# Performance work log

Hardware: AMD Instinct MI355X
Metric: run time of the kernel (lower is better)

The kernel has to match this reference:

```python
import jax, jax.numpy as jnp
import numpy as np

B, Q, K, F, H, D = 2, 4096, 4096, 512, 8, 64

def setup_inputs() -> dict:
    key = jax.random.key(0)
    ks = jax.random.split(key, 6)
    s = 1.0 / np.sqrt(F)
    return {
        "inputs_q": jax.random.normal(ks[0], (B, Q, F), dtype=jnp.float32),
        "inputs_kv": jax.random.normal(ks[1], (B, K, F), dtype=jnp.float32),
        "Wq": jax.random.normal(ks[2], (F, H, D), dtype=jnp.float32) * s,
        "Wk": jax.random.normal(ks[3], (F, H, D), dtype=jnp.float32) * s,
        "Wv": jax.random.normal(ks[4], (F, H, D), dtype=jnp.float32) * s,
        "Wo": jax.random.normal(ks[5], (H, D, F), dtype=jnp.float32) * (1.0 / np.sqrt(H * D)),
    }

def reference(inputs_q, inputs_kv, Wq, Wk, Wv, Wo):
    # QKV projections (DenseGeneral, no bias): [B, L, F] -> [B, L, H, D]
    q = jnp.einsum("bqf,fhd->bqhd", inputs_q, Wq)
    k = jnp.einsum("bkf,fhd->bkhd", inputs_kv, Wk)
    v = jnp.einsum("bkf,fhd->bkhd", inputs_kv, Wv)
    # Explicit attention matrix [B, H, Q, K] as in the original module
    logits = jnp.einsum("bqhd,bkhd->bhqk", q, k)
    attn = jax.nn.softmax(logits, axis=-1)
    out = jnp.einsum("bhqk,bkhd->bqhd", attn, v)
    # Output projection over (heads, head_dim): [B, Q, H, D] -> [B, Q, F]
    return jnp.einsum("bqhd,hdf->bqf", out, Wo)
```

## Files before the change

### kernel.cpp

```cpp
#include <hip/hip_runtime.h>
#include <hip/hip_bf16.h>

typedef short bf16x8 __attribute__((ext_vector_type(8)));
typedef _Float16 f16;
typedef f16 f16x8 __attribute__((ext_vector_type(8)));
typedef float f32x4 __attribute__((ext_vector_type(4)));
typedef unsigned short u16;
typedef u16 u16x8 __attribute__((ext_vector_type(8)));
typedef unsigned int u32;
typedef u32 u32x2 __attribute__((ext_vector_type(2)));

#define B_  2
#define L_  4096
#define F_  512
#define H_  8
#define D_  64
#define M_  8192
#define NSPL 2
#define KHALF (L_ / NSPL)

#define LOG2E 1.442695041f

__device__ inline u16 f2bf(float f) {
    union { float f; unsigned u; } v; v.f = f;
    unsigned r = v.u + 0x7fff + ((v.u >> 16) & 1);
    return (u16)(r >> 16);
}
__device__ inline u16 f2h(float f) {
    union { f16 h; u16 u; } v; v.h = (f16)f;
    return v.u;
}
__device__ inline float h2f(u16 u) {
    union { u16 u; f16 h; } v; v.u = u;
    return (float)v.h;
}

__global__ __launch_bounds__(256) void wt_kernel(
    const float* __restrict__ Wq, const float* __restrict__ Wk,
    const float* __restrict__ Wv, const float* __restrict__ Wo,
    u16* __restrict__ Tq, u16* __restrict__ Tk,
    u16* __restrict__ Tv, u16* __restrict__ To) {
    __shared__ float t[32][33];
    const int z = blockIdx.z;
    const float* in = (z == 0) ? Wq : (z == 1) ? Wk : (z == 2) ? Wv : Wo;
    u16* out = (z == 0) ? Tq : (z == 1) ? Tk : (z == 2) ? Tv : To;
    int k0 = blockIdx.y * 32, n0 = blockIdx.x * 32;
    int c = threadIdx.x & 31, r8 = threadIdx.x >> 5;
#pragma unroll
    for (int i = 0; i < 4; ++i) {
        int r = r8 * 4 + i;
        t[r][c] = in[(size_t)(k0 + r) * F_ + n0 + c];
    }
    __syncthreads();
#pragma unroll
    for (int i = 0; i < 4; ++i) {
        int r = r8 * 4 + i;
        out[(size_t)(n0 + r) * F_ + k0 + c] = f2h(t[c][r]);
    }
}

__global__ __launch_bounds__(256, 3) void proj_kernel(
    const float* __restrict__ Xq, const float* __restrict__ Xkv,
    const u16* __restrict__ Wqt, const u16* __restrict__ Wkt,
    const u16* __restrict__ Wvt,
    u16* __restrict__ Qw, u16* __restrict__ Kw, u16* __restrict__ Vw) {
    __shared__ u16 Ah[128][72];
    __shared__ u16 B1[64][72];
    __shared__ u16 B2[64][72];
    const int tid = threadIdx.x;
    const int w = tid >> 6, lane = tid & 63, lx = lane & 15, quad = lane >> 4;
    const int m0 = blockIdx.y * 128, n0 = blockIdx.x * 64;
    const bool isKV = (blockIdx.z == 1);
    const float* A = isKV ? Xkv : Xq;
    const u16* W1 = isKV ? Wkt : Wqt;

    float4 apre[8];
    u16x8 b1p[2], b2p[2];

    auto load_ab = [&](int k0) {
#pragma unroll
        for (int it = 0; it < 4; ++it) {
            int slot = tid + it * 256, r = slot >> 3, g = (slot & 7) * 8;
            apre[2 * it]     = *(const float4*)(A + (size_t)(m0 + r) * F_ + k0 + g);
            apre[2 * it + 1] = *(const float4*)(A + (size_t)(m0 + r) * F_ + k0 + g + 4);
        }
#pragma unroll
        for (int it = 0; it < 2; ++it) {
            int slot = tid + it * 256, r = slot >> 3, g = (slot & 7) * 8;
            b1p[it] = *(const u16x8*)(W1 + (size_t)(n0 + r) * F_ + k0 + g);
            if (isKV)
                b2p[it] = *(const u16x8*)(Wvt + (size_t)(n0 + r) * F_ + k0 + g);
        }
    };
    auto write_ab = [&]() {
#pragma unroll
        for (int it = 0; it < 4; ++it) {
            int slot = tid + it * 256, r = slot >> 3, g = (slot & 7) * 8;
            float4 f0 = apre[2 * it], f1 = apre[2 * it + 1];
            u16 th[8] = {f2h(f0.x), f2h(f0.y), f2h(f0.z), f2h(f0.w),
                         f2h(f1.x), f2h(f1.y), f2h(f1.z), f2h(f1.w)};
            *(u16x8*)&Ah[r][g] = *(u16x8*)th;
        }
#pragma unroll
        for (int it = 0; it < 2; ++it) {
            int slot = tid + it * 256, r = slot >> 3, g = (slot & 7) * 8;
            *(u16x8*)&B1[r][g] = b1p[it];
            if (isKV) *(u16x8*)&B2[r][g] = b2p[it];
        }
    };

    f32x4 acc1[2][4] = {}, acc2[2][4] = {};

    load_ab(0);
    write_ab();
    __syncthreads();
    load_ab(64);

    for (int k0 = 0; k0 < F_; k0 += 64) {
#pragma unroll
        for (int ks = 0; ks < 2; ++ks) {
            f16x8 af[2];
#pragma unroll
            for (int mf = 0; mf < 2; ++mf)
                af[mf] = *(const f16x8*)&Ah[w * 32 + mf * 16 + lx][ks * 32 + quad * 8];
#pragma unroll
            for (int nt = 0; nt < 4; ++nt) {
                f16x8 b1 = *(const f16x8*)&B1[nt * 16 + lx][ks * 32 + quad * 8];
#pragma unroll
                for (int mf = 0; mf < 2; ++mf)
                    acc1[mf][nt] = __builtin_amdgcn_mfma_f32_16x16x32_f16(af[mf], b1, acc1[mf][nt], 0, 0, 0);
                if (isKV) {
                    f16x8 b2 = *(const f16x8*)&B2[nt * 16 + lx][ks * 32 + quad * 8];
#pragma unroll
                    for (int mf = 0; mf < 2; ++mf)
                        acc2[mf][nt] = __builtin_amdgcn_mfma_f32_16x16x32_f16(af[mf], b2, acc2[mf][nt], 0, 0, 0);
                }
            }
        }
        if (k0 < F_ - 64) {
            __syncthreads();
            write_ab();
            __syncthreads();
            if (k0 < F_ - 128) load_ab(k0 + 128);
        }
    }

    const int h = n0 >> 6;
    const float scl = isKV ? 1.0f : LOG2E;
    u16* C1 = isKV ? Kw : Qw;
#pragma unroll
    for (int mf = 0; mf < 2; ++mf)
#pragma unroll
        for (int nt = 0; nt < 4; ++nt)
#pragma unroll
            for (int i = 0; i < 4; ++i) {
                int m = m0 + w * 32 + mf * 16 + quad * 4 + i;
                int b = m >> 12, l = m & 4095;
                int d = nt * 16 + lx;
                C1[((size_t)(b * H_ + h) * L_ + l) * D_ + d] = f2h(acc1[mf][nt][i] * scl);
            }
    if (isKV) {
        __syncthreads();
#pragma unroll
        for (int mf = 0; mf < 2; ++mf)
#pragma unroll
            for (int nt = 0; nt < 4; ++nt)
#pragma unroll
                for (int i = 0; i < 4; ++i)
                    Ah[w * 32 + mf * 16 + quad * 4 + i][nt * 16 + lx] = f2bf(acc2[mf][nt][i]);
        __syncthreads();
        int d = tid >> 2, seg = (tid & 3) * 32;
        int b = m0 >> 12;
        u16 tmp[32];
#pragma unroll
        for (int j = 0; j < 32; ++j) tmp[j] = Ah[seg + j][d];
        size_t base = ((size_t)(b * H_ + h) * D_ + d) * L_ + (m0 & 4095) + seg;
#pragma unroll
        for (int c = 0; c < 4; ++c)
            *(u16x8*)(Vw + base + c * 8) = *(u16x8*)&tmp[c * 8];
    }
}

__global__ __launch_bounds__(256) void out_gemm(const u16* __restrict__ A16,
                                                const u16* __restrict__ Wt,
                                                float* __restrict__ Cf) {
    __shared__ u16 As[128][72];
    __shared__ u16 Bs[64][72];
    const int tid = threadIdx.x;
    const int w = tid >> 6, lane = tid & 63, lx = lane & 15, quad = lane >> 4;
    const int m0 = blockIdx.y * 128, n0 = blockIdx.x * 64;

    u16x8 a16p[4];
    u16x8 bp[2];

    auto load_ab = [&](int k0) {
#pragma unroll
        for (int it = 0; it < 4; ++it) {
            int slot = tid + it * 256, r = slot >> 3, g = (slot & 7) * 8;
            a16p[it] = *(const u16x8*)(A16 + (size_t)(m0 + r) * F_ + k0 + g);
        }
#pragma unroll
        for (int it = 0; it < 2; ++it) {
            int slot = tid + it * 256, r = slot >> 3, g = (slot & 7) * 8;
            bp[it] = *(const u16x8*)(Wt + (size_t)(n0 + r) * F_ + k0 + g);
        }
    };
    auto write_ab = [&]() {
#pragma unroll
        for (int it = 0; it < 4; ++it) {
            int slot = tid + it * 256, r = slot >> 3, g = (slot & 7) * 8;
            *(u16x8*)&As[r][g] = a16p[it];
        }
#pragma unroll
        for (int it = 0; it < 2; ++it) {
            int slot = tid + it * 256, r = slot >> 3, g = (slot & 7) * 8;
            *(u16x8*)&Bs[r][g] = bp[it];
        }
    };

    f32x4 acc[2][4] = {};

    load_ab(0);
    write_ab();
    __syncthreads();
    load_ab(64);

    for (int k0 = 0; k0 < F_; k0 += 64) {
#pragma unroll
        for (int ks = 0; ks < 2; ++ks) {
            f16x8 af[2];
#pragma unroll
            for (int mf = 0; mf < 2; ++mf)
                af[mf] = *(const f16x8*)&As[w * 32 + mf * 16 + lx][ks * 32 + quad * 8];
#pragma unroll
            for (int nt = 0; nt < 4; ++nt) {
                f16x8 bf = *(const f16x8*)&Bs[nt * 16 + lx][ks * 32 + quad * 8];
#pragma unroll
                for (int mf = 0; mf < 2; ++mf)
                    acc[mf][nt] = __builtin_amdgcn_mfma_f32_16x16x32_f16(af[mf], bf, acc[mf][nt], 0, 0, 0);
            }
        }
        if (k0 < F_ - 64) {
            __syncthreads();
            write_ab();
            __syncthreads();
            if (k0 < F_ - 128) load_ab(k0 + 128);
        }
    }

#pragma unroll
    for (int mf = 0; mf < 2; ++mf)
#pragma unroll
        for (int nt = 0; nt < 4; ++nt)
#pragma unroll
            for (int i = 0; i < 4; ++i) {
                int m = m0 + w * 32 + mf * 16 + quad * 4 + i;
                int n = n0 + nt * 16 + lx;
                Cf[(size_t)m * F_ + n] = acc[mf][nt][i];
            }
}

__global__ __launch_bounds__(256, 2) void flash_mfma(
    const u16* __restrict__ Qg, const u16* __restrict__ Kg,
    const u16* __restrict__ Vtg, u16* __restrict__ On, float* __restrict__ Ls) {
    __shared__ u16 Ks[2][64][72];
    __shared__ u16 Vs[2][64][72];

    const int tid = threadIdx.x;
    const int w = tid >> 6, lane = tid & 63, lx = lane & 15, quad = lane >> 4;

    const int x = blockIdx.x;
    const int t = x >> 3;
    const int hh = t >> 5;
    const int s = (t >> 4) & 1;
    const int bh = (x & 7) * 2 + hh;
    const int q0 = (t & 15) * 256;

    const u16* Qp = Qg + ((size_t)bh * L_ + q0) * D_;
    const u16* Kp = Kg + (size_t)bh * L_ * D_ + (size_t)(s * KHALF) * D_;
    const u16* Vp = Vtg + (size_t)bh * D_ * L_ + s * KHALF;

    f16x8 qreg[4][2];
#pragma unroll
    for (int qf = 0; qf < 4; ++qf)
#pragma unroll
        for (int ks = 0; ks < 2; ++ks)
            qreg[qf][ks] = *(const f16x8*)(Qp + (size_t)(w * 64 + qf * 16 + lx) * D_ +
                                           ks * 32 + quad * 8);

    u16x8 kp[2], vp[2];
    auto load_kv = [&](int kt) {
#pragma unroll
        for (int it = 0; it < 2; ++it) {
            int slot = tid + it * 256, r = slot >> 3, g = (slot & 7) * 8;
            kp[it] = *(const u16x8*)(Kp + (size_t)(kt * 64 + r) * D_ + g);
            vp[it] = *(const u16x8*)(Vp + (size_t)r * L_ + kt * 64 + g);
        }
    };
    auto write_kv = [&](int p) {
#pragma unroll
        for (int it = 0; it < 2; ++it) {
            int slot = tid + it * 256, r = slot >> 3, g = (slot & 7) * 8;
            *(u16x8*)&Ks[p][r][g] = kp[it];
            *(u16x8*)&Vs[p][r][g] = vp[it];
        }
    };

    const bf16x8 vone = {0x3F80, 0x3F80, 0x3F80, 0x3F80,
                         0x3F80, 0x3F80, 0x3F80, 0x3F80};
    f32x4 o[4][4] = {};
    f32x4 osum[4] = {};

    load_kv(0);
    write_kv(0);
    __syncthreads();
    load_kv(1);

    const int NT = KHALF / 64;
    for (int kt = 0; kt < NT; ++kt) {
        const int p = kt & 1;

        f32x4 sv[2][4] = {};
#pragma unroll
        for (int ks = 0; ks < 2; ++ks)
#pragma unroll
            for (int nt = 0; nt < 2; ++nt) {
                f16x8 ak = *(const f16x8*)&Ks[p][nt * 16 + lx][ks * 32 + quad * 8];
#pragma unroll
                for (int qf = 0; qf < 4; ++qf)
                    sv[nt][qf] = __builtin_amdgcn_mfma_f32_16x16x32_f16(ak, qreg[qf][ks], sv[nt][qf], 0, 0, 0);
            }

        if (kt < NT - 1) write_kv(p ^ 1);

        bf16x8 ap0[4];
#pragma unroll
        for (int qf = 0; qf < 4; ++qf) {
            u32 pu[2], pw[2];
#pragma unroll
            for (int nt = 0; nt < 2; ++nt) {
                u32 ub[4];
#pragma unroll
                for (int i = 0; i < 4; ++i)
                    ub[i] = __float_as_uint(__builtin_amdgcn_exp2f(sv[nt][qf][i]));
                pu[nt] = __builtin_amdgcn_perm(ub[1], ub[0], 0x07060302u);
                pw[nt] = __builtin_amdgcn_perm(ub[3], ub[2], 0x07060302u);
            }
            u32x2 r  = __builtin_amdgcn_permlane32_swap(pu[0], pu[1], false, false);
            u32x2 r2 = __builtin_amdgcn_permlane16_swap(r[0], r[1], false, false);
            u32x2 tt = __builtin_amdgcn_permlane32_swap(pw[0], pw[1], false, false);
            u32x2 t2 = __builtin_amdgcn_permlane16_swap(tt[0], tt[1], false, false);
            union { u32 d[4]; bf16x8 h; } cvt;
            cvt.d[0] = r2[0];
            cvt.d[1] = t2[0];
            cvt.d[2] = r2[1];
            cvt.d[3] = t2[1];
            ap0[qf] = cvt.h;
        }

        __builtin_amdgcn_s_setprio(1);
#pragma unroll
        for (int qf = 0; qf < 4; ++qf)
            osum[qf] = __builtin_amdgcn_mfma_f32_16x16x32_bf16(ap0[qf], vone, osum[qf], 0, 0, 0);
#pragma unroll
        for (int nt = 0; nt < 4; ++nt) {
            bf16x8 bv = *(const bf16x8*)&Vs[p][nt * 16 + lx][quad * 8];
#pragma unroll
            for (int qf = 0; qf < 4; ++qf)
                o[qf][nt] = __builtin_amdgcn_mfma_f32_16x16x32_bf16(ap0[qf], bv, o[qf][nt], 0, 0, 0);
        }
        __builtin_amdgcn_s_setprio(0);

#pragma unroll
        for (int nt = 0; nt < 2; ++nt)
#pragma unroll
            for (int qf = 0; qf < 4; ++qf)
                sv[nt][qf] = (f32x4){0.f, 0.f, 0.f, 0.f};
#pragma unroll
        for (int ks = 0; ks < 2; ++ks)
#pragma unroll
            for (int nt = 0; nt < 2; ++nt) {
                f16x8 ak = *(const f16x8*)&Ks[p][(nt + 2) * 16 + lx][ks * 32 + quad * 8];
#pragma unroll
                for (int qf = 0; qf < 4; ++qf)
                    sv[nt][qf] = __builtin_amdgcn_mfma_f32_16x16x32_f16(ak, qreg[qf][ks], sv[nt][qf], 0, 0, 0);
            }

        bf16x8 ap1[4];
#pragma unroll
        for (int qf = 0; qf < 4; ++qf) {
            u32 pu[2], pw[2];
#pragma unroll
            for (int nt = 0; nt < 2; ++nt) {
                u32 ub[4];
#pragma unroll
                for (int i = 0; i < 4; ++i)
                    ub[i] = __float_as_uint(__builtin_amdgcn_exp2f(sv[nt][qf][i]));
                pu[nt] = __builtin_amdgcn_perm(ub[1], ub[0], 0x07060302u);
                pw[nt] = __builtin_amdgcn_perm(ub[3], ub[2], 0x07060302u);
            }
            u32x2 r  = __builtin_amdgcn_permlane32_swap(pu[0], pu[1], false, false);
            u32x2 r2 = __builtin_amdgcn_permlane16_swap(r[0], r[1], false, false);
            u32x2 tt = __builtin_amdgcn_permlane32_swap(pw[0], pw[1], false, false);
            u32x2 t2 = __builtin_amdgcn_permlane16_swap(tt[0], tt[1], false, false);
            union { u32 d[4]; bf16x8 h; } cvt;
            cvt.d[0] = r2[0];
            cvt.d[1] = t2[0];
            cvt.d[2] = r2[1];
            cvt.d[3] = t2[1];
            ap1[qf] = cvt.h;
        }

        __builtin_amdgcn_s_setprio(1);
#pragma unroll
        for (int qf = 0; qf < 4; ++qf)
            osum[qf] = __builtin_amdgcn_mfma_f32_16x16x32_bf16(ap1[qf], vone, osum[qf], 0, 0, 0);
#pragma unroll
        for (int nt = 0; nt < 4; ++nt) {
            bf16x8 bv = *(const bf16x8*)&Vs[p][nt * 16 + lx][32 + quad * 8];
#pragma unroll
            for (int qf = 0; qf < 4; ++qf)
                o[qf][nt] = __builtin_amdgcn_mfma_f32_16x16x32_bf16(ap1[qf], bv, o[qf][nt], 0, 0, 0);
        }
        __builtin_amdgcn_s_setprio(0);

        if (kt < NT - 2) load_kv(kt + 2);
        if (kt < NT - 1) __syncthreads();
    }

    const int b = bh >> 3, h = bh & 7;
    u16* Op = On + (size_t)s * M_ * F_;
#pragma unroll
    for (int qf = 0; qf < 4; ++qf) {
        float linv[4];
#pragma unroll
        for (int i = 0; i < 4; ++i) linv[i] = 1.f / osum[qf][i];
#pragma unroll
        for (int nt = 0; nt < 4; ++nt)
#pragma unroll
            for (int i = 0; i < 4; ++i) {
                int l = q0 + w * 64 + qf * 16 + quad * 4 + i;
                Op[((size_t)b * L_ + l) * (H_ * D_) + h * D_ + nt * 16 + lx] =
                    f2h(o[qf][nt][i] * linv[i]);
            }
        if (lx == 0) {
            float* lp = Ls + ((size_t)s * (B_ * H_) + bh) * L_ +
                        q0 + w * 64 + qf * 16 + quad * 4;
#pragma unroll
            for (int i = 0; i < 4; ++i) lp[i] = osum[qf][i];
        }
    }
}

__global__ __launch_bounds__(256) void reduce_kernel(
    const u16* __restrict__ On, const float* __restrict__ Ls,
    u16* __restrict__ Ow) {
    int gid = blockIdx.x * 256 + threadIdx.x;
    size_t off = (size_t)gid * 8;
    int row = gid >> 3;
    int b = row >> 15, rem = row & 32767;
    int l = rem >> 3, h = rem & 7;
    int lidx = ((b * H_ + h) << 12) + l;
    float l1 = Ls[lidx], l2 = Ls[B_ * H_ * L_ + lidx];
    float w1 = l1 / (l1 + l2), w2 = 1.f - w1;
    u16x8 a = *(const u16x8*)(On + off);
    u16x8 c = *(const u16x8*)(On + (size_t)M_ * F_ + off);
    u16 r[8];
#pragma unroll
    for (int j = 0; j < 8; ++j)
        r[j] = f2h(w1 * h2f(a[j]) + w2 * h2f(c[j]));
    *(u16x8*)(Ow + off) = *(u16x8*)r;
}

extern "C" void kernel_launch(void* const* d_in, const int* in_sizes, int n_in,
                              void* d_out, int out_size, void* d_ws, size_t ws_size,
                              hipStream_t stream)
{
    const float* Xq  = (const float*)d_in[0];
    const float* Xkv = (const float*)d_in[1];
    const float* Wq  = (const float*)d_in[2];
    const float* Wk  = (const float*)d_in[3];
    const float* Wv  = (const float*)d_in[4];
    const float* Wo  = (const float*)d_in[5];
    float* out = (float*)d_out;

    u16* ws  = (u16*)d_ws;
    const size_t MF = (size_t)M_ * F_;
    const size_t FF = (size_t)F_ * F_;
    u16* Wqt = ws;
    u16* Wkt = Wqt + FF;
    u16* Wvt = Wkt + FF;
    u16* Wot = Wvt + FF;
    u16* Qw  = Wot + FF;
    u16* Kw  = Qw + MF;
    u16* Vw  = Kw + MF;
    u16* On  = Vw + MF;
    float* Ls = (float*)(On + 2 * MF);
    u16* Ow  = Qw;

    wt_kernel<<<dim3(16, 16, 4), 256, 0, stream>>>(Wq, Wk, Wv, Wo,
                                                   Wqt, Wkt, Wvt, Wot);

    proj_kernel<<<dim3(8, 64, 2), 256, 0, stream>>>(Xq, Xkv, Wqt, Wkt, Wvt,
                                                    Qw, Kw, Vw);

    flash_mfma<<<dim3(512), 256, 0, stream>>>(Qw, Kw, Vw, On, Ls);

    reduce_kernel<<<dim3((int)(MF / 8 / 256)), 256, 0, stream>>>(On, Ls, Ow);

    out_gemm<<<dim3(8, 64), 256, 0, stream>>>(Ow, Wot, out);
}
```

Before: 215.9 us.

## Load K/V fragments directly from global into registers, bypassing LDS

Drops the shared-memory double buffer for K and V tiles in the flash attention kernel. Each wave now loads its MFMA operand fragments straight from global memory into a register double buffer, and the loop is unrolled by two to alternate buffers. This removes the LDS writes and reads and the per-tile __syncthreads. In exchange, every wave fetches the whole K/V tile itself, multiplying cache traffic by the wave count, and it adds many live vector registers that could cause spills or lower occupancy.

```diff
diff --git a/kernel.cpp b/kernel.cpp
--- a/kernel.cpp
+++ b/kernel.cpp
@@ -263,9 +263,6 @@
 __global__ __launch_bounds__(256, 2) void flash_mfma(
     const u16* __restrict__ Qg, const u16* __restrict__ Kg,
     const u16* __restrict__ Vtg, u16* __restrict__ On, float* __restrict__ Ls) {
-    __shared__ u16 Ks[2][64][72];
-    __shared__ u16 Vs[2][64][72];
-
     const int tid = threadIdx.x;
     const int w = tid >> 6, lane = tid & 63, lx = lane & 15, quad = lane >> 4;
 
@@ -288,22 +285,28 @@
             qreg[qf][ks] = *(const f16x8*)(Qp + (size_t)(w * 64 + qf * 16 + lx) * D_ +
                                            ks * 32 + quad * 8);
 
-    u16x8 kp[2], vp[2];
-    auto load_kv = [&](int kt) {
-#pragma unroll
-        for (int it = 0; it < 2; ++it) {
-            int slot = tid + it * 256, r = slot >> 3, g = (slot & 7) * 8;
-            kp[it] = *(const u16x8*)(Kp + (size_t)(kt * 64 + r) * D_ + g);
-            vp[it] = *(const u16x8*)(Vp + (size_t)r * L_ + kt * 64 + g);
-        }
-    };
-    auto write_kv = [&](int p) {
-#pragma unroll
-        for (int it = 0; it < 2; ++it) {
-            int slot = tid + it * 256, r = slot >> 3, g = (slot & 7) * 8;
-            *(u16x8*)&Ks[p][r][g] = kp[it];
-            *(u16x8*)&Vs[p][r][g] = vp[it];
-        }
+    const u16* kbase = Kp + (size_t)lx * D_ + quad * 8;
+    const u16* vbase = Vp + (size_t)lx * L_ + quad * 8;
+
+    u16x8 k0f[2][4], v0f[2][4], k1f[2][4], v1f[2][4];
+
+    auto load_k = [&](u16x8 (&kd)[2][4], int kt) {
+#pragma unroll
+        for (int h = 0; h < 2; ++h)
+#pragma unroll
+            for (int n = 0; n < 2; ++n)
+#pragma unroll
+                for (int ks = 0; ks < 2; ++ks)
+                    kd[h][n * 2 + ks] = *(const u16x8*)(kbase +
+                        (size_t)(kt * 64 + (h * 2 + n) * 16) * D_ + ks * 32);
+    };
+    auto load_v = [&](u16x8 (&vd)[2][4], int kt) {
+#pragma unroll
+        for (int ks = 0; ks < 2; ++ks)
+#pragma unroll
+            for (int n = 0; n < 4; ++n)
+                vd[ks][n] = *(const u16x8*)(vbase +
+                    (size_t)(n * 16) * L_ + kt * 64 + ks * 32);
     };
 
     const bf16x8 vone = {0x3F80, 0x3F80, 0x3F80, 0x3F80,
@@ -311,40 +314,30 @@
     f32x4 o[4][4] = {};
     f32x4 osum[4] = {};
 
-    load_kv(0);
-    write_kv(0);
-    __syncthreads();
-    load_kv(1);
-
-    const int NT = KHALF / 64;
-    for (int kt = 0; kt < NT; ++kt) {
-        const int p = kt & 1;
-
+    auto halftile = [&](const u16x8 (&kc)[4], const u16x8 (&vc)[4]) {
         f32x4 sv[2][4] = {};
 #pragma unroll
         for (int ks = 0; ks < 2; ++ks)
 #pragma unroll
-            for (int nt = 0; nt < 2; ++nt) {
-                f16x8 ak = *(const f16x8*)&Ks[p][nt * 16 + lx][ks * 32 + quad * 8];
+            for (int n = 0; n < 2; ++n) {
+                f16x8 ak = __builtin_bit_cast(f16x8, kc[n * 2 + ks]);
 #pragma unroll
                 for (int qf = 0; qf < 4; ++qf)
-                    sv[nt][qf] = __builtin_amdgcn_mfma_f32_16x16x32_f16(ak, qreg[qf][ks], sv[nt][qf], 0, 0, 0);
-            }
-
-        if (kt < NT - 1) write_kv(p ^ 1);
-
-        bf16x8 ap0[4];
+                    sv[n][qf] = __builtin_amdgcn_mfma_f32_16x16x32_f16(ak, qreg[qf][ks], sv[n][qf], 0, 0, 0);
+            }
+
+        bf16x8 ap[4];
 #pragma unroll
         for (int qf = 0; qf < 4; ++qf) {
             u32 pu[2], pw[2];
 #pragma unroll
-            for (int nt = 0; nt < 2; ++nt) {
+            for (int n = 0; n < 2; ++n) {
                 u32 ub[4];
 #pragma unroll
                 for (int i = 0; i < 4; ++i)
-                    ub[i] = __float_as_uint(__builtin_amdgcn_exp2f(sv[nt][qf][i]));
-                pu[nt] = __builtin_amdgcn_perm(ub[1], ub[0], 0x07060302u);
-                pw[nt] = __builtin_amdgcn_perm(ub[3], ub[2], 0x07060302u);
+                    ub[i] = __float_as_uint(__builtin_amdgcn_exp2f(sv[n][qf][i]));
+                pu[n] = __builtin_amdgcn_perm(ub[1], ub[0], 0x07060302u);
+                pw[n] = __builtin_amdgcn_perm(ub[3], ub[2], 0x07060302u);
             }
             u32x2 r  = __builtin_amdgcn_permlane32_swap(pu[0], pu[1], false, false);
             u32x2 r2 = __builtin_amdgcn_permlane16_swap(r[0], r[1], false, false);
@@ -355,77 +348,39 @@
             cvt.d[1] = t2[0];
             cvt.d[2] = r2[1];
             cvt.d[3] = t2[1];
-            ap0[qf] = cvt.h;
+            ap[qf] = cvt.h;
         }
 
         __builtin_amdgcn_s_setprio(1);
 #pragma unroll
         for (int qf = 0; qf < 4; ++qf)
-            osum[qf] = __builtin_amdgcn_mfma_f32_16x16x32_bf16(ap0[qf], vone, osum[qf], 0, 0, 0);
+            osum[qf] = __builtin_amdgcn_mfma_f32_16x16x32_bf16(ap[qf], vone, osum[qf], 0, 0, 0);
 #pragma unroll
         for (int nt = 0; nt < 4; ++nt) {
-            bf16x8 bv = *(const bf16x8*)&Vs[p][nt * 16 + lx][quad * 8];
+            bf16x8 bv = __builtin_bit_cast(bf16x8, vc[nt]);
 #pragma unroll
             for (int qf = 0; qf < 4; ++qf)
-                o[qf][nt] = __builtin_amdgcn_mfma_f32_16x16x32_bf16(ap0[qf], bv, o[qf][nt], 0, 0, 0);
+                o[qf][nt] = __builtin_amdgcn_mfma_f32_16x16x32_bf16(ap[qf], bv, o[qf][nt], 0, 0, 0);
         }
         __builtin_amdgcn_s_setprio(0);
-
-#pragma unroll
-        for (int nt = 0; nt < 2; ++nt)
-#pragma unroll
-            for (int qf = 0; qf < 4; ++qf)
-                sv[nt][qf] = (f32x4){0.f, 0.f, 0.f, 0.f};
-#pragma unroll
-        for (int ks = 0; ks < 2; ++ks)
-#pragma unroll
-            for (int nt = 0; nt < 2; ++nt) {
-                f16x8 ak = *(const f16x8*)&Ks[p][(nt + 2) * 16 + lx][ks * 32 + quad * 8];
-#pragma unroll
-                for (int qf = 0; qf < 4; ++qf)
-                    sv[nt][qf] = __builtin_amdgcn_mfma_f32_16x16x32_f16(ak, qreg[qf][ks], sv[nt][qf], 0, 0, 0);
-            }
-
-        bf16x8 ap1[4];
-#pragma unroll
-        for (int qf = 0; qf < 4; ++qf) {
-            u32 pu[2], pw[2];
-#pragma unroll
-            for (int nt = 0; nt < 2; ++nt) {
-                u32 ub[4];
-#pragma unroll
-                for (int i = 0; i < 4; ++i)
-                    ub[i] = __float_as_uint(__builtin_amdgcn_exp2f(sv[nt][qf][i]));
-                pu[nt] = __builtin_amdgcn_perm(ub[1], ub[0], 0x07060302u);
-                pw[nt] = __builtin_amdgcn_perm(ub[3], ub[2], 0x07060302u);
-            }
-            u32x2 r  = __builtin_amdgcn_permlane32_swap(pu[0], pu[1], false, false);
-            u32x2 r2 = __builtin_amdgcn_permlane16_swap(r[0], r[1], false, false);
-            u32x2 tt = __builtin_amdgcn_permlane32_swap(pw[0], pw[1], false, false);
-            u32x2 t2 = __builtin_amdgcn_permlane16_swap(tt[0], tt[1], false, false);
-            union { u32 d[4]; bf16x8 h; } cvt;
-            cvt.d[0] = r2[0];
-            cvt.d[1] = t2[0];
-            cvt.d[2] = r2[1];
-            cvt.d[3] = t2[1];
-            ap1[qf] = cvt.h;
-        }
-
-        __builtin_amdgcn_s_setprio(1);
-#pragma unroll
-        for (int qf = 0; qf < 4; ++qf)
-            osum[qf] = __builtin_amdgcn_mfma_f32_16x16x32_bf16(ap1[qf], vone, osum[qf], 0, 0, 0);
-#pragma unroll
-        for (int nt = 0; nt < 4; ++nt) {
-            bf16x8 bv = *(const bf16x8*)&Vs[p][nt * 16 + lx][32 + quad * 8];
-#pragma unroll
-            for (int qf = 0; qf < 4; ++qf)
-                o[qf][nt] = __builtin_amdgcn_mfma_f32_16x16x32_bf16(ap1[qf], bv, o[qf][nt], 0, 0, 0);
-        }
-        __builtin_amdgcn_s_setprio(0);
-
-        if (kt < NT - 2) load_kv(kt + 2);
-        if (kt < NT - 1) __syncthreads();
+    };
+
+    const int NT = KHALF / 64;
+
+    load_k(k0f, 0);
+    load_v(v0f, 0);
+
+    auto body = [&](u16x8 (&kc)[2][4], u16x8 (&vc)[2][4],
+                    u16x8 (&kn)[2][4], u16x8 (&vn)[2][4], int kt) {
+        if (kt + 1 < NT) load_k(kn, kt + 1);
+        halftile(kc[0], vc[0]);
+        halftile(kc[1], vc[1]);
+        if (kt + 1 < NT) load_v(vn, kt + 1);
+    };
+
+    for (int kt = 0; kt < NT; kt += 2) {
+        body(k0f, v0f, k1f, v1f, kt);
+        body(k1f, v1f, k0f, v0f, kt + 1);
     }
 
     const int b = bh >> 3, h = bh & 7;
```

After: 298.8 us. 1.38x slower.
